# Performance work log

Hardware: AMD Instinct MI355X
Metric: run time of the kernel (lower is better)

The kernel has to match this reference:

```python
import jax, jax.numpy as jnp
import numpy as np

PI = 3.141592653589793


def _nearest_idx(g, size):
    # PyTorch grid_sample nearest, align_corners=False: unnormalize then round half up
    x = ((g + 1.0) * size - 1.0) / 2.0
    return jnp.clip(jnp.floor(x + 0.5).astype(jnp.int32), 0, size - 1)


def setup_inputs() -> dict:
    key = jax.random.key(0)
    ks = jax.random.split(key, 12)
    B, Q, H, W, C, Cf = 1, 65536, 64, 64, 256, 128
    scale = 4  # HR is 256x256
    inp = {
        'inp_img': jax.random.uniform(ks[0], (B, 3, H, W), jnp.float32),
        'coef': jax.random.normal(ks[1], (B, C, H, W), jnp.float32) * 0.5,
        'freq': jax.random.normal(ks[2], (B, Cf, H, W), jnp.float32) * 0.5,
        'coord': jax.random.uniform(ks[3], (B, Q, 2), jnp.float32, minval=-1.0, maxval=1.0),
        'cell': jnp.full((B, Q, 2), 2.0 / (H * scale), jnp.float32),
        'w_coord_fc': jax.random.normal(ks[4], (128, 2), jnp.float32) * 0.5,
        'w_phase': jax.random.normal(ks[5], (128, 2), jnp.float32) * 0.5,
        'w1': jax.random.normal(ks[6], (256, 256), jnp.float32) * (1.0 / 16.0),
        'b1': jnp.zeros((256,), jnp.float32),
        'w2': jax.random.normal(ks[7], (256, 256), jnp.float32) * (1.0 / 16.0),
        'b2': jnp.zeros((256,), jnp.float32),
        'w3': jax.random.normal(ks[8], (3, 256), jnp.float32) * (1.0 / 16.0),
        'b3': jnp.zeros((3,), jnp.float32),
    }
    return inp


def reference(inp_img, coef, freq, coord, cell, w_coord_fc, w_phase, w1, b1, w2, b2, w3, b3):
    B, C, H, W = coef.shape
    Q = coord.shape[1]
    eps = 1e-6
    rx = 1.0 / H  # 2/H/2
    ry = 1.0 / W
    # 4 local-ensemble offsets in loop order (vx,vy) in {-1,1}x{-1,1}
    offs = jnp.array([[-1.0, -1.0], [-1.0, 1.0], [1.0, -1.0], [1.0, 1.0]], jnp.float32)
    shift = offs * jnp.array([rx, ry], jnp.float32) + eps  # [4,2]
    coord_ = jnp.clip(coord[:, None, :, :] + shift[None, :, None, :], -1.0 + eps, 1.0 - eps)  # [B,4,Q,2]

    # coord channel 0 -> H axis, channel 1 -> W axis (after flip(-1) in torch)
    iy = _nearest_idx(coord_[..., 0], H)  # [B,4,Q]
    ix = _nearest_idx(coord_[..., 1], W)
    lin = iy * W + ix  # [B,4,Q]

    def gather(fmap):  # fmap [B,Cc,H,W] -> [B,4,Q,Cc]
        Cc = fmap.shape[1]
        flat = fmap.reshape(B, Cc, H * W).transpose(0, 2, 1)  # [B,HW,Cc]
        return jax.vmap(lambda f, i: f[i])(flat, lin.reshape(B, -1)).reshape(B, 4, Q, Cc)

    q_coef = gather(coef)   # [B,4,Q,256]
    q_freq = gather(freq)   # [B,4,Q,128]

    # feat_coord at nearest pixel = pixel centers from make_coord
    qc_y = -1.0 + (2.0 * iy.astype(jnp.float32) + 1.0) / H
    qc_x = -1.0 + (2.0 * ix.astype(jnp.float32) + 1.0) / W
    rel0 = (coord[:, None, :, 0] - qc_y) * H  # [B,4,Q]
    rel1 = (coord[:, None, :, 1] - qc_x) * W
    rel_coord = jnp.stack([rel0, rel1], axis=-1)  # [B,4,Q,2]
    rel_cell = cell * jnp.array([H, W], jnp.float32)  # [B,Q,2]

    q_freq = q_freq * jnp.einsum('boqd,kd->boqk', rel_coord, w_coord_fc)
    q_freq = q_freq + jnp.einsum('bqd,kd->bqk', rel_cell, w_phase)[:, None]
    q_freq = jnp.concatenate([jnp.cos(PI * q_freq), jnp.sin(PI * q_freq)], axis=-1)  # [B,4,Q,256]

    x = q_coef * q_freq
    h = jax.nn.relu(jnp.einsum('boqc,dc->boqd', x, w1) + b1)
    h = jax.nn.relu(jnp.einsum('boqc,dc->boqd', h, w2) + b2)
    preds = jnp.einsum('boqc,dc->boqd', h, w3) + b3  # [B,4,Q,3]

    area = jnp.abs(rel0 * rel1) + 1e-9  # [B,4,Q]
    tot = jnp.sum(area, axis=1, keepdims=True)
    weights = area[:, ::-1] / tot  # swap 0<->3, 1<->2
    ret = jnp.sum(preds * weights[..., None], axis=1)  # [B,Q,3]

    # bilinear grid_sample of inp_img, padding_mode='border', align_corners=False
    hi, wi = inp_img.shape[-2:]
    gy = jnp.clip(((coord[..., 0] + 1.0) * hi - 1.0) / 2.0, 0.0, hi - 1.0)
    gx = jnp.clip(((coord[..., 1] + 1.0) * wi - 1.0) / 2.0, 0.0, wi - 1.0)
    y0 = jnp.floor(gy).astype(jnp.int32); x0 = jnp.floor(gx).astype(jnp.int32)
    y1 = jnp.clip(y0 + 1, 0, hi - 1); x1 = jnp.clip(x0 + 1, 0, wi - 1)
    wy = gy - y0.astype(jnp.float32); wx = gx - x0.astype(jnp.float32)
    img_flat = inp_img.reshape(B, 3, hi * wi).transpose(0, 2, 1)  # [B,HW,3]
    g = lambda yy, xx: jax.vmap(lambda f, i: f[i])(img_flat, yy * wi + xx)  # [B,Q,3]
    samp = (g(y0, x0) * ((1 - wy) * (1 - wx))[..., None]
            + g(y0, x1) * ((1 - wy) * wx)[..., None]
            + g(y1, x0) * (wy * (1 - wx))[..., None]
            + g(y1, x1) * (wy * wx)[..., None])
    return ret + samp
```

## Files before the change

kernel.cpp:

```cpp
#include <hip/hip_runtime.h>
#include <math.h>

typedef __bf16 bf16_t;
typedef bf16_t bf16x8 __attribute__((ext_vector_type(8)));
typedef float  f32x4  __attribute__((ext_vector_type(4)));

#define PI_F 3.14159265358979323846f

constexpr int H = 64, W = 64, Q = 65536;
constexpr int C = 256, CF = 128;
constexpr int QPB = 32;
constexpr int ROWS = QPB * 4;
constexpr int PADC = 264;


__global__ void transpose_cvt_kernel(const float* __restrict__ src, bf16_t* __restrict__ dst, int Crows) {
    __shared__ float tile[32][33];
    int bx = blockIdx.x * 32;
    int by = blockIdx.y * 32;
    int tx = threadIdx.x & 31;
    int ty = threadIdx.x >> 5;
#pragma unroll
    for (int i = 0; i < 4; i++) {
        tile[ty + i * 8][tx] = src[(by + ty + i * 8) * 4096 + bx + tx];
    }
    __syncthreads();
#pragma unroll
    for (int i = 0; i < 4; i++) {
        dst[(bx + ty + i * 8) * Crows + by + tx] = (bf16_t)tile[tx][ty + i * 8];
    }
}

__global__ void cvt_w_kernel(const float* __restrict__ w1, const float* __restrict__ w2,
                             bf16_t* __restrict__ w1b, bf16_t* __restrict__ w2b) {
    int i = blockIdx.x * 256 + threadIdx.x;
    w1b[i] = (bf16_t)w1[i];
    w2b[i] = (bf16_t)w2[i];
}

__global__ void pack_tab_kernel(const float* __restrict__ wcf, const float* __restrict__ wph,
                                float4* __restrict__ wtab) {
    int k = threadIdx.x;
    float4 v;
    v.x = wcf[k * 2 + 0]; v.y = wcf[k * 2 + 1];
    v.z = wph[k * 2 + 0]; v.w = wph[k * 2 + 1];
    wtab[k] = v;
}


#define LOADB(dst, Wptr, kb)                                                            \
    {                                                                                   \
        dst[0] = *(const bf16x8*)((Wptr) + (wv * 32 + l15) * 256 + (kb) * 32 + l16 * 8);      \
        dst[1] = *(const bf16x8*)((Wptr) + (wv * 32 + 16 + l15) * 256 + (kb) * 32 + l16 * 8); \
    }

__global__ __launch_bounds__(512, 4)
void lte_fused_kernel(const bf16_t* __restrict__ coefT,
                      const bf16_t* __restrict__ freqT,
                      const bf16_t* __restrict__ w1b,
                      const bf16_t* __restrict__ w2b,
                      const float4* __restrict__ wtab,
                      const float* __restrict__ img,
                      const float* __restrict__ coord,
                      const float* __restrict__ cell,
                      const float* __restrict__ b1,
                      const float* __restrict__ b2,
                      const float* __restrict__ w3,
                      const float* __restrict__ b3,
                      float* __restrict__ out)
{
    extern __shared__ char smem[];
    bf16_t* buf    = (bf16_t*)smem;
    float*  w3s    = (float*)(smem + 67584);
    float*  areaS  = (float*)(smem + 70656);
    float*  predsS = (float*)(smem + 71168);

    const int t    = threadIdx.x;
    const int lane = t & 63;
    const int wv   = t >> 6;
    const int l15  = lane & 15;
    const int l16  = lane >> 4;

    for (int i = t; i < 768; i += 512) w3s[i] = w3[i];

    {
        const int row = t >> 2;
        const int t4  = t & 3;
        const int qL  = row >> 2;
        const int o   = row & 3;
        const int q   = blockIdx.x * QPB + qL;
        const float c0  = coord[q * 2 + 0];
        const float c1  = coord[q * 2 + 1];
        const float rc0 = cell[q * 2 + 0] * (float)H;
        const float rc1 = cell[q * 2 + 1] * (float)W;
        const float vx = (o & 2) ? 1.f : -1.f;
        const float vy = (o & 1) ? 1.f : -1.f;
        const float EPS = 1e-6f;
        float g0 = fminf(fmaxf(c0 + vx * (1.f / H) + EPS, -1.f + EPS), 1.f - EPS);
        float g1 = fminf(fmaxf(c1 + vy * (1.f / W) + EPS, -1.f + EPS), 1.f - EPS);
        int iy = (int)floorf(((g0 + 1.f) * (float)H - 1.f) * 0.5f + 0.5f);
        iy = min(max(iy, 0), H - 1);
        int ix = (int)floorf(((g1 + 1.f) * (float)W - 1.f) * 0.5f + 0.5f);
        ix = min(max(ix, 0), W - 1);
        const float rel0 = (c0 - (-1.f + (2.f * (float)iy + 1.f) / (float)H)) * (float)H;
        const float rel1 = (c1 - (-1.f + (2.f * (float)ix + 1.f) / (float)W)) * (float)W;
        if (t4 == 0) areaS[row] = fabsf(rel0 * rel1) + 1e-9f;
        const int pix = iy * W + ix;
        const bf16_t* fq = freqT + pix * CF;
        const bf16_t* cf = coefT + pix * C;
        const int k0 = t4 * 32;

        bf16x8 fqv[4], ccv[4], csv[4];
#pragma unroll
        for (int i = 0; i < 4; i++) {
            fqv[i] = *(const bf16x8*)(fq + k0 + i * 8);
            ccv[i] = *(const bf16x8*)(cf + k0 + i * 8);
            csv[i] = *(const bf16x8*)(cf + 128 + k0 + i * 8);
        }
#pragma unroll
        for (int i = 0; i < 4; i++) {
            bf16x8 vc, vs;
#pragma unroll
            for (int j = 0; j < 8; j++) {
                const int k = k0 + i * 8 + j;
                const float4 tv = wtab[k];
                const float proj = rel0 * tv.x + rel1 * tv.y;
                const float ph   = rc0 * tv.z + rc1 * tv.w;
                const float m = (float)fqv[i][j] * proj + ph;
                float s, cst;
                __sincosf(PI_F * m, &s, &cst);
                vc[j] = (bf16_t)((float)ccv[i][j] * cst);
                vs[j] = (bf16_t)((float)csv[i][j] * s);
            }
            *(bf16x8*)(buf + row * PADC + k0 + i * 8)       = vc;
            *(bf16x8*)(buf + row * PADC + 128 + k0 + i * 8) = vs;
        }
    }

    bf16x8 b1q[8][2];
    LOADB(b1q[0], w1b, 0);
    LOADB(b1q[1], w1b, 1);
    __syncthreads();

    bf16x8 b2q[8][2];
    {
        f32x4 acc[8][2];
#pragma unroll
        for (int mi = 0; mi < 8; mi++)
#pragma unroll
            for (int nf = 0; nf < 2; nf++) {
                f32x4 z = {0.f, 0.f, 0.f, 0.f};
                acc[mi][nf] = z;
            }
#pragma unroll
        for (int kb = 0; kb < 8; kb++) {
            if (kb < 6) { LOADB(b1q[kb + 2], w1b, kb + 2); }
            bf16x8 a[8];
#pragma unroll
            for (int mi = 0; mi < 8; mi++)
                a[mi] = *(bf16x8*)(buf + (mi * 16 + l15) * PADC + kb * 32 + l16 * 8);
#pragma unroll
            for (int mi = 0; mi < 8; mi++)
#pragma unroll
                for (int nf = 0; nf < 2; nf++)
                    acc[mi][nf] = __builtin_amdgcn_mfma_f32_16x16x32_bf16(a[mi], b1q[kb][nf], acc[mi][nf], 0, 0, 0);
        }
        LOADB(b2q[0], w2b, 0);
        LOADB(b2q[1], w2b, 1);
        __syncthreads();
#pragma unroll
        for (int nf = 0; nf < 2; nf++) {
            const int col = wv * 32 + nf * 16 + l15;
            const float bv = b1[col];
#pragma unroll
            for (int mi = 0; mi < 8; mi++)
#pragma unroll
                for (int r = 0; r < 4; r++) {
                    const int row = mi * 16 + l16 * 4 + r;
                    buf[row * PADC + col] = (bf16_t)fmaxf(acc[mi][nf][r] + bv, 0.f);
                }
        }
        __syncthreads();
    }

    {
        f32x4 acc[8][2];
#pragma unroll
        for (int mi = 0; mi < 8; mi++)
#pragma unroll
            for (int nf = 0; nf < 2; nf++) {
                f32x4 z = {0.f, 0.f, 0.f, 0.f};
                acc[mi][nf] = z;
            }
#pragma unroll
        for (int kb = 0; kb < 8; kb++) {
            if (kb < 6) { LOADB(b2q[kb + 2], w2b, kb + 2); }
            bf16x8 a[8];
#pragma unroll
            for (int mi = 0; mi < 8; mi++)
                a[mi] = *(bf16x8*)(buf + (mi * 16 + l15) * PADC + kb * 32 + l16 * 8);
#pragma unroll
            for (int mi = 0; mi < 8; mi++)
#pragma unroll
                for (int nf = 0; nf < 2; nf++)
                    acc[mi][nf] = __builtin_amdgcn_mfma_f32_16x16x32_bf16(a[mi], b2q[kb][nf], acc[mi][nf], 0, 0, 0);
        }
        __syncthreads();
#pragma unroll
        for (int nf = 0; nf < 2; nf++) {
            const int col = wv * 32 + nf * 16 + l15;
            const float bv = b2[col];
#pragma unroll
            for (int mi = 0; mi < 8; mi++)
#pragma unroll
                for (int r = 0; r < 4; r++) {
                    const int row = mi * 16 + l16 * 4 + r;
                    buf[row * PADC + col] = (bf16_t)fmaxf(acc[mi][nf][r] + bv, 0.f);
                }
        }
        __syncthreads();
    }

    {
        const int row = t >> 2;
        const int t4  = t & 3;
        float p0 = 0.f, p1 = 0.f, p2 = 0.f;
#pragma unroll
        for (int c8 = 0; c8 < 8; c8++) {
            const int c = t4 * 64 + c8 * 8;
            bf16x8 hv = *(bf16x8*)(buf + row * PADC + c);
#pragma unroll
            for (int j = 0; j < 8; j++) {
                const float h = (float)hv[j];
                p0 = fmaf(h, w3s[c + j], p0);
                p1 = fmaf(h, w3s[256 + c + j], p1);
                p2 = fmaf(h, w3s[512 + c + j], p2);
            }
        }
        p0 += __shfl_xor(p0, 1); p0 += __shfl_xor(p0, 2);
        p1 += __shfl_xor(p1, 1); p1 += __shfl_xor(p1, 2);
        p2 += __shfl_xor(p2, 1); p2 += __shfl_xor(p2, 2);
        if (t4 == 0) {
            predsS[row * 3 + 0] = p0 + b3[0];
            predsS[row * 3 + 1] = p1 + b3[1];
            predsS[row * 3 + 2] = p2 + b3[2];
        }
    }
    __syncthreads();

    if (t < QPB) {
        const int qL = t;
        const int q  = blockIdx.x * QPB + qL;
        const int r0 = qL * 4;
        const float a0 = areaS[r0 + 0], a1 = areaS[r0 + 1], a2 = areaS[r0 + 2], a3 = areaS[r0 + 3];
        const float inv = 1.f / (a0 + a1 + a2 + a3);
        const float wgt0 = a3 * inv, wgt1 = a2 * inv, wgt2 = a1 * inv, wgt3 = a0 * inv;
        const float c0 = coord[q * 2 + 0];
        const float c1 = coord[q * 2 + 1];
        float gy = fminf(fmaxf(((c0 + 1.f) * (float)H - 1.f) * 0.5f, 0.f), (float)(H - 1));
        float gx = fminf(fmaxf(((c1 + 1.f) * (float)W - 1.f) * 0.5f, 0.f), (float)(W - 1));
        int y0 = (int)floorf(gy); int x0 = (int)floorf(gx);
        int y1 = min(y0 + 1, H - 1); int x1 = min(x0 + 1, W - 1);
        const float wy = gy - (float)y0, wx = gx - (float)x0;
#pragma unroll
        for (int ch = 0; ch < 3; ch++) {
            const float ret = predsS[(r0 + 0) * 3 + ch] * wgt0 + predsS[(r0 + 1) * 3 + ch] * wgt1
                            + predsS[(r0 + 2) * 3 + ch] * wgt2 + predsS[(r0 + 3) * 3 + ch] * wgt3;
            const float* ip = img + ch * 4096;
            const float v00 = ip[y0 * 64 + x0], v01 = ip[y0 * 64 + x1];
            const float v10 = ip[y1 * 64 + x0], v11 = ip[y1 * 64 + x1];
            const float samp = v00 * (1.f - wy) * (1.f - wx) + v01 * (1.f - wy) * wx
                             + v10 * wy * (1.f - wx) + v11 * wy * wx;
            out[q * 3 + ch] = ret + samp;
        }
    }
}


extern "C" void kernel_launch(void* const* d_in, const int* in_sizes, int n_in,
                              void* d_out, int out_size, void* d_ws, size_t ws_size,
                              hipStream_t stream) {
    const float* img   = (const float*)d_in[0];
    const float* coef  = (const float*)d_in[1];
    const float* freq  = (const float*)d_in[2];
    const float* coord = (const float*)d_in[3];
    const float* cell  = (const float*)d_in[4];
    const float* wcf   = (const float*)d_in[5];
    const float* wph   = (const float*)d_in[6];
    const float* w1    = (const float*)d_in[7];
    const float* b1    = (const float*)d_in[8];
    const float* w2    = (const float*)d_in[9];
    const float* b2    = (const float*)d_in[10];
    const float* w3    = (const float*)d_in[11];
    const float* b3    = (const float*)d_in[12];
    float* out = (float*)d_out;

    char* ws = (char*)d_ws;
    bf16_t* coefT = (bf16_t*)ws;
    bf16_t* freqT = (bf16_t*)(ws + 2097152);
    bf16_t* w1b   = (bf16_t*)(ws + 3145728);
    bf16_t* w2b   = (bf16_t*)(ws + 3276800);
    float4* wtab  = (float4*)(ws + 3407872);

    transpose_cvt_kernel<<<dim3(128, 8), 256, 0, stream>>>(coef, coefT, 256);
    transpose_cvt_kernel<<<dim3(128, 4), 256, 0, stream>>>(freq, freqT, 128);
    cvt_w_kernel<<<256, 256, 0, stream>>>(w1, w2, w1b, w2b);
    pack_tab_kernel<<<1, 128, 0, stream>>>(wcf, wph, wtab);

    const size_t ldsBytes = 72704;
    lte_fused_kernel<<<Q / QPB, 512, ldsBytes, stream>>>(
        coefT, freqT, w1b, w2b, wtab, img, coord, cell, b1, b2, w3, b3, out);
}
```

Before: 194.0 us.

## Retile MLP GEMMs to 2x4 wave grid, move final layer to MFMA

The 8 waves now tile the 128x256 hidden GEMMs as a 2x4 grid (64 rows by 64 columns each) instead of each wave covering all 128 rows by 32 columns. This halves the A-fragment LDS reads per wave, and a 2-deep register double buffer replaces the 8-deep B prefetch, which lowers register pressure. The last 256->3 layer becomes an MFMA over a zero-padded bf16 w3 built by a new prep kernel, replacing the scalar FMA loop and shuffle reduction. The trade-off is a larger B fetch per wave from global memory, plus one extra small kernel launch.

```diff
diff --git a/kernel.cpp b/kernel.cpp
--- a/kernel.cpp
+++ b/kernel.cpp
@@ -10,7 +10,6 @@
 constexpr int H = 64, W = 64, Q = 65536;
 constexpr int C = 256, CF = 128;
 constexpr int QPB = 32;
-constexpr int ROWS = QPB * 4;
 constexpr int PADC = 264;
 
 
@@ -21,14 +20,12 @@
     int tx = threadIdx.x & 31;
     int ty = threadIdx.x >> 5;
 #pragma unroll
-    for (int i = 0; i < 4; i++) {
+    for (int i = 0; i < 4; i++)
         tile[ty + i * 8][tx] = src[(by + ty + i * 8) * 4096 + bx + tx];
-    }
     __syncthreads();
 #pragma unroll
-    for (int i = 0; i < 4; i++) {
+    for (int i = 0; i < 4; i++)
         dst[(bx + ty + i * 8) * Crows + by + tx] = (bf16_t)tile[tx][ty + i * 8];
-    }
 }
 
 __global__ void cvt_w_kernel(const float* __restrict__ w1, const float* __restrict__ w2,
@@ -47,41 +44,47 @@
     wtab[k] = v;
 }
 
-
-#define LOADB(dst, Wptr, kb)                                                            \
-    {                                                                                   \
-        dst[0] = *(const bf16x8*)((Wptr) + (wv * 32 + l15) * 256 + (kb) * 32 + l16 * 8);      \
-        dst[1] = *(const bf16x8*)((Wptr) + (wv * 32 + 16 + l15) * 256 + (kb) * 32 + l16 * 8); \
-    }
+__global__ void cvt_w3_kernel(const float* __restrict__ w3, bf16_t* __restrict__ w3p) {
+    int k = threadIdx.x;
+#pragma unroll
+    for (int n = 0; n < 16; n++)
+        w3p[n * 256 + k] = (n < 3) ? (bf16_t)w3[n * 256 + k] : (bf16_t)0.f;
+}
+
+
+#define LOADB4(dst, Wptr, kb) {                                                             \
+    dst[0] = *(const bf16x8*)((Wptr) + (wc * 64 +  0 + l15) * 256 + (kb) * 32 + l16 * 8);   \
+    dst[1] = *(const bf16x8*)((Wptr) + (wc * 64 + 16 + l15) * 256 + (kb) * 32 + l16 * 8);   \
+    dst[2] = *(const bf16x8*)((Wptr) + (wc * 64 + 32 + l15) * 256 + (kb) * 32 + l16 * 8);   \
+    dst[3] = *(const bf16x8*)((Wptr) + (wc * 64 + 48 + l15) * 256 + (kb) * 32 + l16 * 8); }
 
 __global__ __launch_bounds__(512, 4)
 void lte_fused_kernel(const bf16_t* __restrict__ coefT,
                       const bf16_t* __restrict__ freqT,
                       const bf16_t* __restrict__ w1b,
                       const bf16_t* __restrict__ w2b,
+                      const bf16_t* __restrict__ w3p,
                       const float4* __restrict__ wtab,
                       const float* __restrict__ img,
                       const float* __restrict__ coord,
                       const float* __restrict__ cell,
                       const float* __restrict__ b1,
                       const float* __restrict__ b2,
-                      const float* __restrict__ w3,
                       const float* __restrict__ b3,
                       float* __restrict__ out)
 {
     extern __shared__ char smem[];
     bf16_t* buf    = (bf16_t*)smem;
-    float*  w3s    = (float*)(smem + 67584);
-    float*  areaS  = (float*)(smem + 70656);
-    float*  predsS = (float*)(smem + 71168);
+    float*  areaS  = (float*)(smem + 67584);
+    float*  predsS = (float*)(smem + 68096);
 
     const int t    = threadIdx.x;
     const int lane = t & 63;
     const int wv   = t >> 6;
+    const int wr   = wv >> 2;
+    const int wc   = wv & 3;
     const int l15  = lane & 15;
     const int l16  = lane >> 4;
-
-    for (int i = t; i < 768; i += 512) w3s[i] = w3[i];
 
     {
         const int row = t >> 2;
@@ -137,46 +140,44 @@
         }
     }
 
-    bf16x8 b1q[8][2];
-    LOADB(b1q[0], w1b, 0);
-    LOADB(b1q[1], w1b, 1);
+    bf16x8 bq[2][4];
+    LOADB4(bq[0], w1b, 0);
     __syncthreads();
 
-    bf16x8 b2q[8][2];
+    bf16x8 cq[2][4];
     {
-        f32x4 acc[8][2];
-#pragma unroll
-        for (int mi = 0; mi < 8; mi++)
-#pragma unroll
-            for (int nf = 0; nf < 2; nf++) {
+        f32x4 acc[4][4];
+#pragma unroll
+        for (int mi = 0; mi < 4; mi++)
+#pragma unroll
+            for (int nf = 0; nf < 4; nf++) {
                 f32x4 z = {0.f, 0.f, 0.f, 0.f};
                 acc[mi][nf] = z;
             }
 #pragma unroll
         for (int kb = 0; kb < 8; kb++) {
-            if (kb < 6) { LOADB(b1q[kb + 2], w1b, kb + 2); }
-            bf16x8 a[8];
-#pragma unroll
-            for (int mi = 0; mi < 8; mi++)
-                a[mi] = *(bf16x8*)(buf + (mi * 16 + l15) * PADC + kb * 32 + l16 * 8);
-#pragma unroll
-            for (int mi = 0; mi < 8; mi++)
-#pragma unroll
-                for (int nf = 0; nf < 2; nf++)
-                    acc[mi][nf] = __builtin_amdgcn_mfma_f32_16x16x32_bf16(a[mi], b1q[kb][nf], acc[mi][nf], 0, 0, 0);
-        }
-        LOADB(b2q[0], w2b, 0);
-        LOADB(b2q[1], w2b, 1);
+            if (kb < 7) { LOADB4(bq[(kb + 1) & 1], w1b, kb + 1); }
+            bf16x8 a[4];
+#pragma unroll
+            for (int mi = 0; mi < 4; mi++)
+                a[mi] = *(bf16x8*)(buf + (wr * 64 + mi * 16 + l15) * PADC + kb * 32 + l16 * 8);
+#pragma unroll
+            for (int mi = 0; mi < 4; mi++)
+#pragma unroll
+                for (int nf = 0; nf < 4; nf++)
+                    acc[mi][nf] = __builtin_amdgcn_mfma_f32_16x16x32_bf16(a[mi], bq[kb & 1][nf], acc[mi][nf], 0, 0, 0);
+        }
+        LOADB4(cq[0], w2b, 0);
         __syncthreads();
 #pragma unroll
-        for (int nf = 0; nf < 2; nf++) {
-            const int col = wv * 32 + nf * 16 + l15;
+        for (int nf = 0; nf < 4; nf++) {
+            const int col = wc * 64 + nf * 16 + l15;
             const float bv = b1[col];
 #pragma unroll
-            for (int mi = 0; mi < 8; mi++)
+            for (int mi = 0; mi < 4; mi++)
 #pragma unroll
                 for (int r = 0; r < 4; r++) {
-                    const int row = mi * 16 + l16 * 4 + r;
+                    const int row = wr * 64 + mi * 16 + l16 * 4 + r;
                     buf[row * PADC + col] = (bf16_t)fmaxf(acc[mi][nf][r] + bv, 0.f);
                 }
         }
@@ -184,37 +185,37 @@
     }
 
     {
-        f32x4 acc[8][2];
-#pragma unroll
-        for (int mi = 0; mi < 8; mi++)
-#pragma unroll
-            for (int nf = 0; nf < 2; nf++) {
+        f32x4 acc[4][4];
+#pragma unroll
+        for (int mi = 0; mi < 4; mi++)
+#pragma unroll
+            for (int nf = 0; nf < 4; nf++) {
                 f32x4 z = {0.f, 0.f, 0.f, 0.f};
                 acc[mi][nf] = z;
             }
 #pragma unroll
         for (int kb = 0; kb < 8; kb++) {
-            if (kb < 6) { LOADB(b2q[kb + 2], w2b, kb + 2); }
-            bf16x8 a[8];
-#pragma unroll
-            for (int mi = 0; mi < 8; mi++)
-                a[mi] = *(bf16x8*)(buf + (mi * 16 + l15) * PADC + kb * 32 + l16 * 8);
-#pragma unroll
-            for (int mi = 0; mi < 8; mi++)
-#pragma unroll
-                for (int nf = 0; nf < 2; nf++)
-                    acc[mi][nf] = __builtin_amdgcn_mfma_f32_16x16x32_bf16(a[mi], b2q[kb][nf], acc[mi][nf], 0, 0, 0);
+            if (kb < 7) { LOADB4(cq[(kb + 1) & 1], w2b, kb + 1); }
+            bf16x8 a[4];
+#pragma unroll
+            for (int mi = 0; mi < 4; mi++)
+                a[mi] = *(bf16x8*)(buf + (wr * 64 + mi * 16 + l15) * PADC + kb * 32 + l16 * 8);
+#pragma unroll
+            for (int mi = 0; mi < 4; mi++)
+#pragma unroll
+                for (int nf = 0; nf < 4; nf++)
+                    acc[mi][nf] = __builtin_amdgcn_mfma_f32_16x16x32_bf16(a[mi], cq[kb & 1][nf], acc[mi][nf], 0, 0, 0);
         }
         __syncthreads();
 #pragma unroll
-        for (int nf = 0; nf < 2; nf++) {
-            const int col = wv * 32 + nf * 16 + l15;
+        for (int nf = 0; nf < 4; nf++) {
+            const int col = wc * 64 + nf * 16 + l15;
             const float bv = b2[col];
 #pragma unroll
-            for (int mi = 0; mi < 8; mi++)
+            for (int mi = 0; mi < 4; mi++)
 #pragma unroll
                 for (int r = 0; r < 4; r++) {
-                    const int row = mi * 16 + l16 * 4 + r;
+                    const int row = wr * 64 + mi * 16 + l16 * 4 + r;
                     buf[row * PADC + col] = (bf16_t)fmaxf(acc[mi][nf][r] + bv, 0.f);
                 }
         }
@@ -222,28 +223,20 @@
     }
 
     {
-        const int row = t >> 2;
-        const int t4  = t & 3;
-        float p0 = 0.f, p1 = 0.f, p2 = 0.f;
-#pragma unroll
-        for (int c8 = 0; c8 < 8; c8++) {
-            const int c = t4 * 64 + c8 * 8;
-            bf16x8 hv = *(bf16x8*)(buf + row * PADC + c);
-#pragma unroll
-            for (int j = 0; j < 8; j++) {
-                const float h = (float)hv[j];
-                p0 = fmaf(h, w3s[c + j], p0);
-                p1 = fmaf(h, w3s[256 + c + j], p1);
-                p2 = fmaf(h, w3s[512 + c + j], p2);
+        f32x4 acc3 = {0.f, 0.f, 0.f, 0.f};
+#pragma unroll
+        for (int kb = 0; kb < 8; kb++) {
+            bf16x8 a = *(bf16x8*)(buf + (wv * 16 + l15) * PADC + kb * 32 + l16 * 8);
+            bf16x8 b = *(const bf16x8*)(w3p + l15 * 256 + kb * 32 + l16 * 8);
+            acc3 = __builtin_amdgcn_mfma_f32_16x16x32_bf16(a, b, acc3, 0, 0, 0);
+        }
+        if (l15 < 3) {
+            const float bv = b3[l15];
+#pragma unroll
+            for (int r = 0; r < 4; r++) {
+                const int row = wv * 16 + l16 * 4 + r;
+                predsS[row * 3 + l15] = acc3[r] + bv;
             }
-        }
-        p0 += __shfl_xor(p0, 1); p0 += __shfl_xor(p0, 2);
-        p1 += __shfl_xor(p1, 1); p1 += __shfl_xor(p1, 2);
-        p2 += __shfl_xor(p2, 1); p2 += __shfl_xor(p2, 2);
-        if (t4 == 0) {
-            predsS[row * 3 + 0] = p0 + b3[0];
-            predsS[row * 3 + 1] = p1 + b3[1];
-            predsS[row * 3 + 2] = p2 + b3[2];
         }
     }
     __syncthreads();
@@ -301,13 +294,15 @@
     bf16_t* w1b   = (bf16_t*)(ws + 3145728);
     bf16_t* w2b   = (bf16_t*)(ws + 3276800);
     float4* wtab  = (float4*)(ws + 3407872);
+    bf16_t* w3p   = (bf16_t*)(ws + 3409920);
 
     transpose_cvt_kernel<<<dim3(128, 8), 256, 0, stream>>>(coef, coefT, 256);
     transpose_cvt_kernel<<<dim3(128, 4), 256, 0, stream>>>(freq, freqT, 128);
     cvt_w_kernel<<<256, 256, 0, stream>>>(w1, w2, w1b, w2b);
     pack_tab_kernel<<<1, 128, 0, stream>>>(wcf, wph, wtab);
-
-    const size_t ldsBytes = 72704;
+    cvt_w3_kernel<<<1, 256, 0, stream>>>(w3, w3p);
+
+    const size_t ldsBytes = 69632;
     lte_fused_kernel<<<Q / QPB, 512, ldsBytes, stream>>>(
-        coefT, freqT, w1b, w2b, wtab, img, coord, cell, b1, b2, w3, b3, out);
-}
+        coefT, freqT, w1b, w2b, w3p, wtab, img, coord, cell, b1, b2, b3, out);
+}
```

Result: slower. 219.6 us (+13.2%).
